# Optimization experiments

Hardware: AMD Instinct MI355X
Metric: run time of the kernel (lower is better)

Reference implementation:

```python
import jax, jax.numpy as jnp
import numpy as np

B, N, T_OBS, T_S, D, D_H, P = 32, 256, 50, 25, 128, 256, 8
TWO_PI = 2.0 * np.pi
EPS = 1e-4


def setup_inputs() -> dict:
    key = jax.random.key(0)
    ks = jax.random.split(key, 12)
    s = 0.02
    return {
        "x_ego_mean": jax.random.normal(ks[0], (B, T_OBS, 2), jnp.float32),
        "x_nei_mean": jax.random.normal(ks[1], (B, N, T_OBS, 2), jnp.float32),
        "f_ego": jax.random.normal(ks[2], (B, T_S, D), jnp.float32),
        "f_nei": jax.random.normal(ks[3], (B, N, T_S, D), jnp.float32),
        "W1": s * jax.random.normal(ks[4], (D, D_H), jnp.float32),
        "b1": jnp.zeros((D_H,), jnp.float32),
        "W2": s * jax.random.normal(ks[5], (D_H, D_H), jnp.float32),
        "b2": jnp.zeros((D_H,), jnp.float32),
        "W3": s * jax.random.normal(ks[6], (D_H, D // 2), jnp.float32),
        "b3": jnp.zeros((D // 2,), jnp.float32),
        "Wce": s * jax.random.normal(ks[7], (2, D // 2), jnp.float32),
        "bce": jnp.zeros((D // 2,), jnp.float32),
    }


def reference(x_ego_mean, x_nei_mean, f_ego, f_nei, W1, b1, W2, b2, W3, b3, Wce, bce):
    # --- spectral-similarity feature branch ---
    fn = f_ego[..., None, :, :] * f_nei            # [B, N, T_s, D]
    fn = jnp.max(fn, axis=-3)                      # max over neighbors -> [B, T_s, D]
    h = jax.nn.relu(fn @ W1 + b1)
    h = jax.nn.relu(h @ W2 + b2)
    fn = jax.nn.relu(h @ W3 + b3)                  # [B, T_s, D//2]

    # --- angle-based partitioning of relative positions ---
    t_r = int(np.ceil(x_ego_mean.shape[-2] / f_ego.shape[-2]))  # static stride
    p_nei = x_nei_mean - x_ego_mean[..., None, :, :]            # [B, N, T_obs, 2]
    p_nei = p_nei[..., ::t_r, :]                                # [B, N, T_s, 2]
    f_distance = jnp.linalg.norm(p_nei, axis=-1)                # [B, N, T_s]
    f_angle = jnp.mod(jnp.arctan2(p_nei[..., 0], p_nei[..., 1]), TWO_PI)
    pidx = (f_angle / (TWO_PI / P)).astype(jnp.int32)           # [B, N, T_s]

    nei_mask = (jnp.sum(jnp.abs(p_nei), axis=-1) != 0).astype(jnp.int32)
    non_self_mask = (f_distance > 0.005).astype(jnp.int32)
    final_mask = nei_mask * non_self_mask
    pidx = pidx * final_mask + (-1) * (1 - final_mask)          # invalid -> -1

    # one-hot over partitions replaces the per-partition python loop
    onehot = (pidx[..., None] == jnp.arange(P, dtype=jnp.int32)).astype(f_distance.dtype)  # [B,N,T_s,P]
    counts = jnp.sum(onehot, axis=-3)                           # [B, T_s, P]
    n = counts + EPS
    dist_mean = jnp.sum(f_distance[..., None] * onehot, axis=-3) / n   # [B, T_s, P]
    ang_mean = jnp.sum(f_angle[..., None] * onehot, axis=-3) / n       # [B, T_s, P]

    # original: y_p = sum_N(fn * mask)/n; fn has no N dim, so this is fn * counts / n
    y = fn[..., :, None, :] * (counts / n)[..., None]           # [B, T_s, P, D//2]

    positions = jnp.stack([dist_mean, ang_mean], axis=-1)       # [B, T_s, P, 2]
    pos_enc = jax.nn.relu(positions @ Wce + bce)                # [B, T_s, P, D//2]
    return jnp.concatenate([y, pos_enc], axis=-1)               # [B, T_s, P, D]
```

## Files before the change

### kernel.cpp

```cpp
#include <hip/hip_runtime.h>
#include <math.h>
#include <float.h>

#define B_ 32
#define N_ 256
#define T_OBS_ 50
#define T_S_ 25
#define D_ 128
#define D_H_ 256
#define P_ 8
#define NCH_ 8
#define NPC_ (N_ / NCH_)
#define PLANE_ (T_S_ * D_)
#define RB_ 2

static constexpr double TWO_PI_D = 6.283185307179586476925286766559;
static constexpr float EPS_F = 1e-4f;

__global__ __launch_bounds__(800) void k1_partial(
    const float* __restrict__ f_ego, const float* __restrict__ f_nei,
    float* __restrict__ part) {
  int b = blockIdx.x >> 3;
  int c = blockIdx.x & 7;
  int tid = threadIdx.x;
  int t = tid >> 5;
  int d4 = tid & 31;

  const float4 e =
      *(const float4*)(f_ego + ((size_t)b * T_S_ + t) * D_ + 4 * d4);
  const float* base =
      f_nei + ((size_t)b * N_ + (size_t)c * NPC_) * PLANE_ + 4 * tid;

  float4 m = make_float4(-FLT_MAX, -FLT_MAX, -FLT_MAX, -FLT_MAX);
#pragma unroll 8
  for (int i = 0; i < NPC_; ++i) {
    float4 v = *(const float4*)(base + (size_t)i * PLANE_);
    m.x = fmaxf(m.x, e.x * v.x);
    m.y = fmaxf(m.y, e.y * v.y);
    m.z = fmaxf(m.z, e.z * v.z);
    m.w = fmaxf(m.w, e.w * v.w);
  }
  *(float4*)(part + (size_t)blockIdx.x * PLANE_ + 4 * tid) = m;
}

__global__ __launch_bounds__(512) void k2_fused(
    const float* __restrict__ part, const float* __restrict__ W1,
    const float* __restrict__ b1, const float* __restrict__ W2,
    const float* __restrict__ b2, const float* __restrict__ W3,
    const float* __restrict__ b3, const float* __restrict__ x_ego,
    const float* __restrict__ x_nei, const float* __restrict__ Wce,
    const float* __restrict__ bce, float* __restrict__ out) {
  __shared__ float spool[4096];
  __shared__ float sin_[RB_][D_];
  __shared__ float sh1[RB_][D_H_];
  __shared__ float sh2[RB_][D_H_];
  __shared__ float f3s[RB_][64];
  __shared__ float cnt[RB_][P_], dsum[RB_][P_], asum[RB_][P_];

  const int tid = threadIdx.x;
  const int row0 = blockIdx.x * RB_;

  if (tid < RB_ * P_) {
    (&cnt[0][0])[tid] = 0.f;
    (&dsum[0][0])[tid] = 0.f;
    (&asum[0][0])[tid] = 0.f;
  }

  if (tid < RB_ * D_) {
    int r = tid >> 7, d = tid & 127;
    int row = row0 + r;
    int b = row / T_S_, t = row - b * T_S_;
    const float* p = part + (size_t)b * NCH_ * PLANE_ + t * D_ + d;
    float m = -FLT_MAX;
#pragma unroll
    for (int c = 0; c < NCH_; ++c) m = fmaxf(m, p[(size_t)c * PLANE_]);
    sin_[r][d] = m;
  }

  float2 eg, xn;
  {
    int r = tid >> 8, n = tid & 255;
    int row = row0 + r;
    int b = row / T_S_, t = row - b * T_S_;
    int tobs = 2 * t;
    eg = *(const float2*)&x_ego[((size_t)b * T_OBS_ + tobs) * 2];
    xn = *(const float2*)&x_nei[(((size_t)b * N_ + n) * T_OBS_ + tobs) * 2];
  }

  const float bb1 = b1[tid & 255];
  const float bb2 = b2[tid & 255];

  __syncthreads();

  {
    const int s = tid >> 6, j4 = tid & 63;
    const float4* W1v = (const float4*)W1;
    float a[RB_][4] = {};
#pragma unroll
    for (int kk = 0; kk < 16; ++kk) {
      int k = s * 16 + kk;
      float4 w = W1v[k * 64 + j4];
#pragma unroll
      for (int r = 0; r < RB_; ++r) {
        float x = sin_[r][k];
        a[r][0] = fmaf(x, w.x, a[r][0]);
        a[r][1] = fmaf(x, w.y, a[r][1]);
        a[r][2] = fmaf(x, w.z, a[r][2]);
        a[r][3] = fmaf(x, w.w, a[r][3]);
      }
    }
#pragma unroll
    for (int r = 0; r < RB_; ++r)
      *(float4*)&spool[(s * RB_ + r) * 256 + 4 * j4] =
          make_float4(a[r][0], a[r][1], a[r][2], a[r][3]);
  }
  __syncthreads();
  {
    int r = tid >> 8, j = tid & 255;
    float sum = bb1;
#pragma unroll
    for (int s = 0; s < 8; ++s) sum += spool[(s * RB_ + r) * 256 + j];
    sh1[r][j] = fmaxf(sum, 0.f);
  }
  __syncthreads();

  {
    const int s = tid >> 6, j4 = tid & 63;
    const float4* W2v = (const float4*)W2;
    float a[RB_][4] = {};
#pragma unroll
    for (int kk = 0; kk < 32; ++kk) {
      int k = s * 32 + kk;
      float4 w = W2v[k * 64 + j4];
#pragma unroll
      for (int r = 0; r < RB_; ++r) {
        float x = sh1[r][k];
        a[r][0] = fmaf(x, w.x, a[r][0]);
        a[r][1] = fmaf(x, w.y, a[r][1]);
        a[r][2] = fmaf(x, w.z, a[r][2]);
        a[r][3] = fmaf(x, w.w, a[r][3]);
      }
    }
#pragma unroll
    for (int r = 0; r < RB_; ++r)
      *(float4*)&spool[(s * RB_ + r) * 256 + 4 * j4] =
          make_float4(a[r][0], a[r][1], a[r][2], a[r][3]);
  }
  __syncthreads();
  {
    int r = tid >> 8, j = tid & 255;
    float sum = bb2;
#pragma unroll
    for (int s = 0; s < 8; ++s) sum += spool[(s * RB_ + r) * 256 + j];
    sh2[r][j] = fmaxf(sum, 0.f);
  }
  __syncthreads();

  {
    const int s3 = tid >> 4, j4 = tid & 15;
    const float4* W3v = (const float4*)W3;
    float a[RB_][4] = {};
#pragma unroll
    for (int kk = 0; kk < 8; ++kk) {
      int k = s3 * 8 + kk;
      float4 w = W3v[k * 16 + j4];
#pragma unroll
      for (int r = 0; r < RB_; ++r) {
        float x = sh2[r][k];
        a[r][0] = fmaf(x, w.x, a[r][0]);
        a[r][1] = fmaf(x, w.y, a[r][1]);
        a[r][2] = fmaf(x, w.z, a[r][2]);
        a[r][3] = fmaf(x, w.w, a[r][3]);
      }
    }
#pragma unroll
    for (int r = 0; r < RB_; ++r)
      *(float4*)&spool[(s3 * RB_ + r) * 64 + 4 * j4] =
          make_float4(a[r][0], a[r][1], a[r][2], a[r][3]);
  }
  {
    int r = tid >> 8;
    float p0 = xn.x - eg.x;
    float p1 = xn.y - eg.y;
    float dist = sqrtf(p0 * p0 + p1 * p1);
    double angd = atan2((double)p0, (double)p1);
    if (angd < 0.0) angd += TWO_PI_D;
    float ang = (float)angd;
    int pidx = (int)(angd / (TWO_PI_D / (double)P_));
    bool mask = ((fabsf(p0) + fabsf(p1)) != 0.f) && (dist > 0.005f);
    if (mask && pidx >= 0 && pidx < P_) {
      atomicAdd(&cnt[r][pidx], 1.f);
      atomicAdd(&dsum[r][pidx], dist);
      atomicAdd(&asum[r][pidx], ang);
    }
  }
  __syncthreads();

  if (tid < RB_ * 64) {
    int r = tid >> 6, j = tid & 63;
    float sum = b3[j];
#pragma unroll
    for (int s = 0; s < 32; ++s) sum += spool[(s * RB_ + r) * 64 + j];
    f3s[r][j] = fmaxf(sum, 0.f);
  }
  __syncthreads();

  {
    int r = tid >> 8, i4 = tid & 255;
    int p = i4 >> 5;
    int c0 = (i4 & 31) * 4;
    float nn = cnt[r][p] + EPS_F;
    float4 v;
    if (c0 < 64) {
      float sc = cnt[r][p] / nn;
      v = make_float4(f3s[r][c0 + 0] * sc, f3s[r][c0 + 1] * sc,
                      f3s[r][c0 + 2] * sc, f3s[r][c0 + 3] * sc);
    } else {
      int jj = c0 - 64;
      float dm = dsum[r][p] / nn;
      float am = asum[r][p] / nn;
      v.x = fmaxf(fmaf(dm, Wce[jj + 0], fmaf(am, Wce[64 + jj + 0], bce[jj + 0])), 0.f);
      v.y = fmaxf(fmaf(dm, Wce[jj + 1], fmaf(am, Wce[64 + jj + 1], bce[jj + 1])), 0.f);
      v.z = fmaxf(fmaf(dm, Wce[jj + 2], fmaf(am, Wce[64 + jj + 2], bce[jj + 2])), 0.f);
      v.w = fmaxf(fmaf(dm, Wce[jj + 3], fmaf(am, Wce[64 + jj + 3], bce[jj + 3])), 0.f);
    }
    *(float4*)(out + (size_t)(row0 + r) * 1024 + 4 * i4) = v;
  }
}

extern "C" void kernel_launch(void* const* d_in, const int* in_sizes, int n_in,
                              void* d_out, int out_size, void* d_ws,
                              size_t ws_size, hipStream_t stream) {
  const float* x_ego = (const float*)d_in[0];
  const float* x_nei = (const float*)d_in[1];
  const float* f_ego = (const float*)d_in[2];
  const float* f_nei = (const float*)d_in[3];
  const float* W1 = (const float*)d_in[4];
  const float* b1 = (const float*)d_in[5];
  const float* W2 = (const float*)d_in[6];
  const float* b2 = (const float*)d_in[7];
  const float* W3 = (const float*)d_in[8];
  const float* b3 = (const float*)d_in[9];
  const float* Wce = (const float*)d_in[10];
  const float* bce = (const float*)d_in[11];
  float* out = (float*)d_out;

  float* part = (float*)d_ws;

  k1_partial<<<B_ * NCH_, 800, 0, stream>>>(f_ego, f_nei, part);
  k2_fused<<<(B_ * T_S_) / RB_, 512, 0, stream>>>(part, W1, b1, W2, b2, W3,
                                                  b3, x_ego, x_nei, Wce, bce,
                                                  out);
}
```

Baseline: 38.72 us.

## Fuse neighbor max-reduction into MLP kernel, eliminating partial workspace pass

Merges the two kernels into one. Each block handles one batch and a pair of time steps, computes the max over all 256 neighbors itself through an in-block shared-memory reduction, then runs the MLP and partition stage. This removes the second launch and the global partial buffer round-trip. In exchange, f_nei loads become strided gathers of 512 bytes per neighbor row instead of contiguous planes. The odd last time step is computed twice, so one output row is written redundantly.

```diff
diff --git a/kernel.cpp b/kernel.cpp
--- a/kernel.cpp
+++ b/kernel.cpp
@@ -9,99 +9,98 @@
 #define D_ 128
 #define D_H_ 256
 #define P_ 8
-#define NCH_ 8
-#define NPC_ (N_ / NCH_)
 #define PLANE_ (T_S_ * D_)
-#define RB_ 2
+#define TG_ 13
 
 static constexpr double TWO_PI_D = 6.283185307179586476925286766559;
 static constexpr float EPS_F = 1e-4f;
 
-__global__ __launch_bounds__(800) void k1_partial(
+__global__ __launch_bounds__(512) void fused(
     const float* __restrict__ f_ego, const float* __restrict__ f_nei,
-    float* __restrict__ part) {
-  int b = blockIdx.x >> 3;
-  int c = blockIdx.x & 7;
-  int tid = threadIdx.x;
-  int t = tid >> 5;
-  int d4 = tid & 31;
-
-  const float4 e =
-      *(const float4*)(f_ego + ((size_t)b * T_S_ + t) * D_ + 4 * d4);
-  const float* base =
-      f_nei + ((size_t)b * N_ + (size_t)c * NPC_) * PLANE_ + 4 * tid;
-
-  float4 m = make_float4(-FLT_MAX, -FLT_MAX, -FLT_MAX, -FLT_MAX);
+    const float* __restrict__ W1, const float* __restrict__ b1,
+    const float* __restrict__ W2, const float* __restrict__ b2,
+    const float* __restrict__ W3, const float* __restrict__ b3,
+    const float* __restrict__ x_ego, const float* __restrict__ x_nei,
+    const float* __restrict__ Wce, const float* __restrict__ bce,
+    float* __restrict__ out) {
+  __shared__ float spool[4096];
+  __shared__ float sin_[2][D_];
+  __shared__ float sh1[2][D_H_];
+  __shared__ float sh2[2][D_H_];
+  __shared__ float f3s[2][64];
+  __shared__ float cnt[2][P_], dsum[2][P_], asum[2][P_];
+
+  const int tid = threadIdx.x;
+  const int b = blockIdx.x / TG_;
+  const int g = blockIdx.x - b * TG_;
+  const int t0 = 2 * g;
+  const int t1 = (2 * g + 1 < T_S_) ? (2 * g + 1) : (T_S_ - 1);
+
+  {
+    const int sub = tid & 63;
+    const int lt = sub >> 5;
+    const int d4 = sub & 31;
+    const int ng = tid >> 6;
+    const int t = lt ? t1 : t0;
+    const float4 e =
+        *(const float4*)(f_ego + ((size_t)b * T_S_ + t) * D_ + 4 * d4);
+    const float* base = f_nei + (size_t)b * N_ * PLANE_ + t * D_ + 4 * d4;
+    float4 m = make_float4(-FLT_MAX, -FLT_MAX, -FLT_MAX, -FLT_MAX);
 #pragma unroll 8
-  for (int i = 0; i < NPC_; ++i) {
-    float4 v = *(const float4*)(base + (size_t)i * PLANE_);
-    m.x = fmaxf(m.x, e.x * v.x);
-    m.y = fmaxf(m.y, e.y * v.y);
-    m.z = fmaxf(m.z, e.z * v.z);
-    m.w = fmaxf(m.w, e.w * v.w);
-  }
-  *(float4*)(part + (size_t)blockIdx.x * PLANE_ + 4 * tid) = m;
-}
-
-__global__ __launch_bounds__(512) void k2_fused(
-    const float* __restrict__ part, const float* __restrict__ W1,
-    const float* __restrict__ b1, const float* __restrict__ W2,
-    const float* __restrict__ b2, const float* __restrict__ W3,
-    const float* __restrict__ b3, const float* __restrict__ x_ego,
-    const float* __restrict__ x_nei, const float* __restrict__ Wce,
-    const float* __restrict__ bce, float* __restrict__ out) {
-  __shared__ float spool[4096];
-  __shared__ float sin_[RB_][D_];
-  __shared__ float sh1[RB_][D_H_];
-  __shared__ float sh2[RB_][D_H_];
-  __shared__ float f3s[RB_][64];
-  __shared__ float cnt[RB_][P_], dsum[RB_][P_], asum[RB_][P_];
-
-  const int tid = threadIdx.x;
-  const int row0 = blockIdx.x * RB_;
-
-  if (tid < RB_ * P_) {
+    for (int i = 0; i < 32; ++i) {
+      int n = ng + 8 * i;
+      float4 v = *(const float4*)(base + (size_t)n * PLANE_);
+      m.x = fmaxf(m.x, e.x * v.x);
+      m.y = fmaxf(m.y, e.y * v.y);
+      m.z = fmaxf(m.z, e.z * v.z);
+      m.w = fmaxf(m.w, e.w * v.w);
+    }
+    ((float4*)spool)[ng * 64 + sub] = m;
+  }
+
+  if (tid < 2 * P_) {
     (&cnt[0][0])[tid] = 0.f;
     (&dsum[0][0])[tid] = 0.f;
     (&asum[0][0])[tid] = 0.f;
   }
 
-  if (tid < RB_ * D_) {
-    int r = tid >> 7, d = tid & 127;
-    int row = row0 + r;
-    int b = row / T_S_, t = row - b * T_S_;
-    const float* p = part + (size_t)b * NCH_ * PLANE_ + t * D_ + d;
-    float m = -FLT_MAX;
-#pragma unroll
-    for (int c = 0; c < NCH_; ++c) m = fmaxf(m, p[(size_t)c * PLANE_]);
-    sin_[r][d] = m;
-  }
-
   float2 eg, xn;
   {
     int r = tid >> 8, n = tid & 255;
-    int row = row0 + r;
-    int b = row / T_S_, t = row - b * T_S_;
+    int t = r ? t1 : t0;
     int tobs = 2 * t;
     eg = *(const float2*)&x_ego[((size_t)b * T_OBS_ + tobs) * 2];
     xn = *(const float2*)&x_nei[(((size_t)b * N_ + n) * T_OBS_ + tobs) * 2];
   }
-
   const float bb1 = b1[tid & 255];
   const float bb2 = b2[tid & 255];
 
   __syncthreads();
 
+  if (tid < 64) {
+    float4 r = ((float4*)spool)[tid];
+#pragma unroll
+    for (int ngg = 1; ngg < 8; ++ngg) {
+      float4 v = ((float4*)spool)[ngg * 64 + tid];
+      r.x = fmaxf(r.x, v.x);
+      r.y = fmaxf(r.y, v.y);
+      r.z = fmaxf(r.z, v.z);
+      r.w = fmaxf(r.w, v.w);
+    }
+    *(float4*)&sin_[tid >> 5][4 * (tid & 31)] = r;
+  }
+  __syncthreads();
+
   {
     const int s = tid >> 6, j4 = tid & 63;
     const float4* W1v = (const float4*)W1;
-    float a[RB_][4] = {};
+    float a[2][4] = {};
 #pragma unroll
     for (int kk = 0; kk < 16; ++kk) {
       int k = s * 16 + kk;
       float4 w = W1v[k * 64 + j4];
 #pragma unroll
-      for (int r = 0; r < RB_; ++r) {
+      for (int r = 0; r < 2; ++r) {
         float x = sin_[r][k];
         a[r][0] = fmaf(x, w.x, a[r][0]);
         a[r][1] = fmaf(x, w.y, a[r][1]);
@@ -110,8 +109,8 @@
       }
     }
 #pragma unroll
-    for (int r = 0; r < RB_; ++r)
-      *(float4*)&spool[(s * RB_ + r) * 256 + 4 * j4] =
+    for (int r = 0; r < 2; ++r)
+      *(float4*)&spool[(s * 2 + r) * 256 + 4 * j4] =
           make_float4(a[r][0], a[r][1], a[r][2], a[r][3]);
   }
   __syncthreads();
@@ -119,7 +118,7 @@
     int r = tid >> 8, j = tid & 255;
     float sum = bb1;
 #pragma unroll
-    for (int s = 0; s < 8; ++s) sum += spool[(s * RB_ + r) * 256 + j];
+    for (int s = 0; s < 8; ++s) sum += spool[(s * 2 + r) * 256 + j];
     sh1[r][j] = fmaxf(sum, 0.f);
   }
   __syncthreads();
@@ -127,13 +126,13 @@
   {
     const int s = tid >> 6, j4 = tid & 63;
     const float4* W2v = (const float4*)W2;
-    float a[RB_][4] = {};
+    float a[2][4] = {};
 #pragma unroll
     for (int kk = 0; kk < 32; ++kk) {
       int k = s * 32 + kk;
       float4 w = W2v[k * 64 + j4];
 #pragma unroll
-      for (int r = 0; r < RB_; ++r) {
+      for (int r = 0; r < 2; ++r) {
         float x = sh1[r][k];
         a[r][0] = fmaf(x, w.x, a[r][0]);
         a[r][1] = fmaf(x, w.y, a[r][1]);
@@ -142,8 +141,8 @@
       }
     }
 #pragma unroll
-    for (int r = 0; r < RB_; ++r)
-      *(float4*)&spool[(s * RB_ + r) * 256 + 4 * j4] =
+    for (int r = 0; r < 2; ++r)
+      *(float4*)&spool[(s * 2 + r) * 256 + 4 * j4] =
           make_float4(a[r][0], a[r][1], a[r][2], a[r][3]);
   }
   __syncthreads();
@@ -151,7 +150,7 @@
     int r = tid >> 8, j = tid & 255;
     float sum = bb2;
 #pragma unroll
-    for (int s = 0; s < 8; ++s) sum += spool[(s * RB_ + r) * 256 + j];
+    for (int s = 0; s < 8; ++s) sum += spool[(s * 2 + r) * 256 + j];
     sh2[r][j] = fmaxf(sum, 0.f);
   }
   __syncthreads();
@@ -159,13 +158,13 @@
   {
     const int s3 = tid >> 4, j4 = tid & 15;
     const float4* W3v = (const float4*)W3;
-    float a[RB_][4] = {};
+    float a[2][4] = {};
 #pragma unroll
     for (int kk = 0; kk < 8; ++kk) {
       int k = s3 * 8 + kk;
       float4 w = W3v[k * 16 + j4];
 #pragma unroll
-      for (int r = 0; r < RB_; ++r) {
+      for (int r = 0; r < 2; ++r) {
         float x = sh2[r][k];
         a[r][0] = fmaf(x, w.x, a[r][0]);
         a[r][1] = fmaf(x, w.y, a[r][1]);
@@ -174,8 +173,8 @@
       }
     }
 #pragma unroll
-    for (int r = 0; r < RB_; ++r)
-      *(float4*)&spool[(s3 * RB_ + r) * 64 + 4 * j4] =
+    for (int r = 0; r < 2; ++r)
+      *(float4*)&spool[(s3 * 2 + r) * 64 + 4 * j4] =
           make_float4(a[r][0], a[r][1], a[r][2], a[r][3]);
   }
   {
@@ -196,17 +195,18 @@
   }
   __syncthreads();
 
-  if (tid < RB_ * 64) {
+  if (tid < 2 * 64) {
     int r = tid >> 6, j = tid & 63;
     float sum = b3[j];
 #pragma unroll
-    for (int s = 0; s < 32; ++s) sum += spool[(s * RB_ + r) * 64 + j];
+    for (int s = 0; s < 32; ++s) sum += spool[(s * 2 + r) * 64 + j];
     f3s[r][j] = fmaxf(sum, 0.f);
   }
   __syncthreads();
 
   {
     int r = tid >> 8, i4 = tid & 255;
+    int t = r ? t1 : t0;
     int p = i4 >> 5;
     int c0 = (i4 & 31) * 4;
     float nn = cnt[r][p] + EPS_F;
@@ -224,7 +224,7 @@
       v.z = fmaxf(fmaf(dm, Wce[jj + 2], fmaf(am, Wce[64 + jj + 2], bce[jj + 2])), 0.f);
       v.w = fmaxf(fmaf(dm, Wce[jj + 3], fmaf(am, Wce[64 + jj + 3], bce[jj + 3])), 0.f);
     }
-    *(float4*)(out + (size_t)(row0 + r) * 1024 + 4 * i4) = v;
+    *(float4*)(out + ((size_t)b * T_S_ + t) * 1024 + 4 * i4) = v;
   }
 }
 
@@ -245,10 +245,6 @@
   const float* bce = (const float*)d_in[11];
   float* out = (float*)d_out;
 
-  float* part = (float*)d_ws;
-
-  k1_partial<<<B_ * NCH_, 800, 0, stream>>>(f_ego, f_nei, part);
-  k2_fused<<<(B_ * T_S_) / RB_, 512, 0, stream>>>(part, W1, b1, W2, b2, W3,
-                                                  b3, x_ego, x_nei, Wce, bce,
-                                                  out);
+  fused<<<B_ * TG_, 512, 0, stream>>>(f_ego, f_nei, W1, b1, W2, b2, W3, b3,
+                                      x_ego, x_nei, Wce, bce, out);
 }
```

Result: faster. 34.02 us (-12.2%).
